# Optimization experiments

Measured on AMD Instinct MI355X. Metric: run time of the kernel, lower is better.

## Reference

```python
import jax, jax.numpy as jnp
import numpy as np

N_NODES = 100000
N_EDGES = 800000
IN_FEATS = 128
HIDDEN = 128
NUM_CLASSES = 10
NUM_GRAPHS = 128
BN_EPS = 1e-5


def setup_inputs() -> dict:
    key = jax.random.key(0)
    ks = jax.random.split(key, 16)
    s = 0.05  # weight init scale
    return {
        "x": jax.random.normal(ks[0], (N_NODES, IN_FEATS), dtype=jnp.float32),
        "edge_index": jax.random.randint(ks[1], (2, N_EDGES), 0, N_NODES, dtype=jnp.int64),
        "batch": jnp.sort(jax.random.randint(ks[2], (N_NODES,), 0, NUM_GRAPHS, dtype=jnp.int64)),
        # conv1 MLP: Linear(in,h) -> ReLU -> Linear(h,h)
        "W1a": jax.random.normal(ks[3], (IN_FEATS, HIDDEN), dtype=jnp.float32) * s,
        "b1a": jnp.zeros((HIDDEN,), dtype=jnp.float32),
        "W1b": jax.random.normal(ks[4], (HIDDEN, HIDDEN), dtype=jnp.float32) * s,
        "b1b": jnp.zeros((HIDDEN,), dtype=jnp.float32),
        "gamma1": jnp.ones((HIDDEN,), dtype=jnp.float32),
        "beta1": jnp.zeros((HIDDEN,), dtype=jnp.float32),
        # conv2 MLP
        "W2a": jax.random.normal(ks[5], (HIDDEN, HIDDEN), dtype=jnp.float32) * s,
        "b2a": jnp.zeros((HIDDEN,), dtype=jnp.float32),
        "W2b": jax.random.normal(ks[6], (HIDDEN, HIDDEN), dtype=jnp.float32) * s,
        "b2b": jnp.zeros((HIDDEN,), dtype=jnp.float32),
        "gamma2": jnp.ones((HIDDEN,), dtype=jnp.float32),
        "beta2": jnp.zeros((HIDDEN,), dtype=jnp.float32),
        # final classifier
        "Wlin": jax.random.normal(ks[7], (HIDDEN, NUM_CLASSES), dtype=jnp.float32) * s,
        "blin": jnp.zeros((NUM_CLASSES,), dtype=jnp.float32),
    }


def _gin_conv(x, edge_index, Wa, ba, Wb, bb, eps=0.0):
    # GINConv: MLP((1+eps)*x_i + sum_{j->i} x_j); scatter-add over edges
    src, dst = edge_index[0], edge_index[1]
    agg = jax.ops.segment_sum(x[src], dst, num_segments=N_NODES)
    h = (1.0 + eps) * x + agg
    h = jax.nn.relu(h @ Wa + ba) @ Wb + bb
    return h


def _batch_norm(x, gamma, beta):
    # training-mode BN over the node dim (biased variance, as in torch)
    mean = jnp.mean(x, axis=0)
    var = jnp.mean(jnp.square(x - mean), axis=0)
    return (x - mean) * jax.lax.rsqrt(var + BN_EPS) * gamma + beta


def reference(x, edge_index, batch, W1a, b1a, W1b, b1b, gamma1, beta1,
              W2a, b2a, W2b, b2b, gamma2, beta2, Wlin, blin):
    h = _gin_conv(x, edge_index, W1a, b1a, W1b, b1b)
    h = jax.nn.relu(_batch_norm(h, gamma1, beta1))
    # dropout: eval mode -> identity
    h = _gin_conv(h, edge_index, W2a, b2a, W2b, b2b)
    h = jax.nn.relu(_batch_norm(h, gamma2, beta2))
    # global mean pool per graph
    summed = jax.ops.segment_sum(h, batch, num_segments=NUM_GRAPHS)
    counts = jax.ops.segment_sum(jnp.ones((h.shape[0],), h.dtype), batch, num_segments=NUM_GRAPHS)
    pooled = summed / jnp.maximum(counts, 1.0)[:, None]  # [G, H]
    logits = pooled @ Wlin + blin
    return jax.nn.log_softmax(logits, axis=1)
```

## Files before the change

kernel.cpp:

```cpp
#include <hip/hip_runtime.h>

#define N_NODES 100000
#define N_EDGESC 800000
#define HID 128
#define NGRAPH 128
#define BN_EPS 1e-5f
#define NREP 32
#define PS 136
#define MLP_GRID 521

#define PBLK 256
#define PCHUNK 3125
#define NCOARSE 196
#define HISTN (NCOARSE * PBLK)
#define HSCAN_BLOCKS (HISTN / 1024)

typedef __bf16 bf16x8 __attribute__((ext_vector_type(8)));
typedef float f32x4 __attribute__((ext_vector_type(4)));

__device__ inline unsigned short f2bf(float f) {
    unsigned int u = __float_as_uint(f);
    unsigned int r = u + 0x7FFFu + ((u >> 16) & 1u);
    return (unsigned short)(r >> 16);
}
__device__ inline float b2f(unsigned short u) {
    return __uint_as_float(((unsigned int)u) << 16);
}


__global__ __launch_bounds__(256) void k_phist(const int* __restrict__ dst,
                                               int* __restrict__ hist)
{
    __shared__ int h[NCOARSE];
    if (threadIdx.x < NCOARSE) h[threadIdx.x] = 0;
    __syncthreads();
    int base = blockIdx.x * PCHUNK;
    for (int i = threadIdx.x; i < PCHUNK; i += 256)
        atomicAdd(&h[dst[base + i] >> 9], 1);
    __syncthreads();
    if (threadIdx.x < NCOARSE)
        hist[threadIdx.x * PBLK + blockIdx.x] = h[threadIdx.x];
}

__global__ __launch_bounds__(256) void k_scan_block(int* __restrict__ a,
    int* __restrict__ bsum, int n)
{
    __shared__ int ts[256];
    int base = blockIdx.x * 1024 + threadIdx.x * 4;
    int v[4], s = 0;
    #pragma unroll
    for (int i = 0; i < 4; ++i) {
        int idx = base + i;
        v[i] = (idx < n) ? a[idx] : 0;
        s += v[i];
    }
    ts[threadIdx.x] = s;
    __syncthreads();
    for (int d = 1; d < 256; d <<= 1) {
        int t = (threadIdx.x >= d) ? ts[threadIdx.x - d] : 0;
        __syncthreads();
        ts[threadIdx.x] += t;
        __syncthreads();
    }
    int run = ts[threadIdx.x] - s;
    #pragma unroll
    for (int i = 0; i < 4; ++i) {
        int idx = base + i;
        if (idx < n) a[idx] = run;
        run += v[i];
    }
    if (threadIdx.x == 255) bsum[blockIdx.x] = ts[255];
}

__global__ void k_scan_top(int* __restrict__ bsum, int nb)
{
    int run = 0;
    for (int i = 0; i < nb; ++i) { int t = bsum[i]; bsum[i] = run; run += t; }
}

__global__ __launch_bounds__(256) void k_scan_add(int* __restrict__ a,
    const int* __restrict__ bsum, int n)
{
    int i = blockIdx.x * 256 + threadIdx.x;
    if (i < n) a[i] += bsum[i >> 10];
}

__global__ __launch_bounds__(256) void k_pscatter(const int* __restrict__ src,
    const int* __restrict__ dst, const int* __restrict__ hist,
    unsigned int* __restrict__ pk1)
{
    __shared__ int cur[NCOARSE];
    if (threadIdx.x < NCOARSE)
        cur[threadIdx.x] = hist[threadIdx.x * PBLK + blockIdx.x];
    __syncthreads();
    int base = blockIdx.x * PCHUNK;
    for (int i = threadIdx.x; i < PCHUNK; i += 256) {
        int s = src[base + i], d = dst[base + i];
        int p = atomicAdd(&cur[d >> 9], 1);
        pk1[p] = ((unsigned int)s << 9) | (unsigned int)(d & 511);
    }
}

__global__ __launch_bounds__(256) void k_psort(const unsigned int* __restrict__ pk1,
    const int* __restrict__ hist, int* __restrict__ eidx, int* __restrict__ off)
{
    __shared__ int h[512], cur[512], ts[256];
    const int b = blockIdx.x;
    const int e0 = hist[b * PBLK];
    const int e1 = (b == NCOARSE - 1) ? N_EDGESC : hist[(b + 1) * PBLK];
    const int cnt = e1 - e0;
    h[threadIdx.x] = 0; h[threadIdx.x + 256] = 0;
    __syncthreads();
    for (int i = threadIdx.x; i < cnt; i += 256)
        atomicAdd(&h[pk1[e0 + i] & 511], 1);
    __syncthreads();
    int v0 = h[threadIdx.x * 2], v1 = h[threadIdx.x * 2 + 1];
    int s = v0 + v1;
    ts[threadIdx.x] = s;
    __syncthreads();
    for (int d = 1; d < 256; d <<= 1) {
        int t = (threadIdx.x >= d) ? ts[threadIdx.x - d] : 0;
        __syncthreads();
        ts[threadIdx.x] += t;
        __syncthreads();
    }
    int run = e0 + ts[threadIdx.x] - s;
    int n0 = b * 512 + threadIdx.x * 2;
    cur[threadIdx.x * 2]     = run;
    cur[threadIdx.x * 2 + 1] = run + v0;
    if (n0     <= N_NODES) off[n0]     = run;
    if (n0 + 1 <= N_NODES) off[n0 + 1] = run + v0;
    __syncthreads();
    for (int i = threadIdx.x; i < cnt; i += 256) {
        unsigned int u = pk1[e0 + i];
        int p = atomicAdd(&cur[u & 511], 1);
        eidx[p] = (int)(u >> 9);
    }
}

__global__ __launch_bounds__(256) void k_cvt(const float* __restrict__ X,
    unsigned short* __restrict__ Y, int n4)
{
    int i = blockIdx.x * 256 + threadIdx.x;
    if (i < n4) {
        float4 v = ((const float4*)X)[i];
        ((ushort4*)Y)[i] = make_ushort4(f2bf(v.x), f2bf(v.y), f2bf(v.z), f2bf(v.w));
    }
}

__global__ __launch_bounds__(256) void k_wcvt4(const float* __restrict__ Wa,
    const float* __restrict__ Wb, const float* __restrict__ Wc,
    const float* __restrict__ Wd, unsigned short* __restrict__ WT)
{
    int idx = blockIdx.x * 256 + threadIdx.x;
    int mat = idx >> 14, w = idx & 16383;
    int k = w >> 7, n = w & 127;
    const float* W = (mat == 0) ? Wa : (mat == 1) ? Wb : (mat == 2) ? Wc : Wd;
    WT[mat * 16384 + n * 128 + k] = f2bf(W[w]);
}

template<bool BN>
__device__ inline void acc_row(float* acc, uint4 v,
                               const float* sc, const float* sh)
{
    unsigned int u[4] = {v.x, v.y, v.z, v.w};
    #pragma unroll
    for (int j = 0; j < 4; ++j) {
        float lo = b2f((unsigned short)u[j]);
        float hi = b2f((unsigned short)(u[j] >> 16));
        if (BN) {
            lo = fmaxf(lo * sc[2*j]   + sh[2*j],   0.f);
            hi = fmaxf(hi * sc[2*j+1] + sh[2*j+1], 0.f);
        }
        acc[2*j]   += lo;
        acc[2*j+1] += hi;
    }
}

template<bool BN>
__global__ __launch_bounds__(256) void k_gather(
    const unsigned short* __restrict__ X, const float* __restrict__ SC,
    const int* __restrict__ off, const int* __restrict__ eidx,
    unsigned short* __restrict__ OUT, int M)
{
    int n = blockIdx.x * 16 + (threadIdx.x >> 4);
    if (n >= M) return;
    const int lane = threadIdx.x & 15;
    const size_t co = (size_t)lane * 8;

    float sc[8], sh[8];
    if (BN) {
        *(float4*)&sc[0] = ((const float4*)SC)[lane * 2];
        *(float4*)&sc[4] = ((const float4*)SC)[lane * 2 + 1];
        *(float4*)&sh[0] = ((const float4*)SC)[32 + lane * 2];
        *(float4*)&sh[4] = ((const float4*)SC)[32 + lane * 2 + 1];
    }

    float acc[8] = {0.f, 0.f, 0.f, 0.f, 0.f, 0.f, 0.f, 0.f};
    acc_row<BN>(acc, *(const uint4*)(X + (size_t)n * HID + co), sc, sh);

    int k = off[n], kend = off[n + 1];
    for (; k + 7 < kend; k += 8) {
        uint4 v0 = *(const uint4*)(X + (size_t)eidx[k]   * HID + co);
        uint4 v1 = *(const uint4*)(X + (size_t)eidx[k+1] * HID + co);
        uint4 v2 = *(const uint4*)(X + (size_t)eidx[k+2] * HID + co);
        uint4 v3 = *(const uint4*)(X + (size_t)eidx[k+3] * HID + co);
        uint4 v4 = *(const uint4*)(X + (size_t)eidx[k+4] * HID + co);
        uint4 v5 = *(const uint4*)(X + (size_t)eidx[k+5] * HID + co);
        uint4 v6 = *(const uint4*)(X + (size_t)eidx[k+6] * HID + co);
        uint4 v7 = *(const uint4*)(X + (size_t)eidx[k+7] * HID + co);
        acc_row<BN>(acc, v0, sc, sh); acc_row<BN>(acc, v1, sc, sh);
        acc_row<BN>(acc, v2, sc, sh); acc_row<BN>(acc, v3, sc, sh);
        acc_row<BN>(acc, v4, sc, sh); acc_row<BN>(acc, v5, sc, sh);
        acc_row<BN>(acc, v6, sc, sh); acc_row<BN>(acc, v7, sc, sh);
    }
    for (; k + 3 < kend; k += 4) {
        uint4 v0 = *(const uint4*)(X + (size_t)eidx[k]   * HID + co);
        uint4 v1 = *(const uint4*)(X + (size_t)eidx[k+1] * HID + co);
        uint4 v2 = *(const uint4*)(X + (size_t)eidx[k+2] * HID + co);
        uint4 v3 = *(const uint4*)(X + (size_t)eidx[k+3] * HID + co);
        acc_row<BN>(acc, v0, sc, sh); acc_row<BN>(acc, v1, sc, sh);
        acc_row<BN>(acc, v2, sc, sh); acc_row<BN>(acc, v3, sc, sh);
    }
    for (; k < kend; ++k) {
        uint4 v = *(const uint4*)(X + (size_t)eidx[k] * HID + co);
        acc_row<BN>(acc, v, sc, sh);
    }

    uint4 o;
    o.x = (unsigned int)f2bf(acc[0]) | ((unsigned int)f2bf(acc[1]) << 16);
    o.y = (unsigned int)f2bf(acc[2]) | ((unsigned int)f2bf(acc[3]) << 16);
    o.z = (unsigned int)f2bf(acc[4]) | ((unsigned int)f2bf(acc[5]) << 16);
    o.w = (unsigned int)f2bf(acc[6]) | ((unsigned int)f2bf(acc[7]) << 16);
    *(uint4*)(OUT + (size_t)n * HID + co) = o;
}

__global__ __launch_bounds__(256) void k_mlp(
    const unsigned short* __restrict__ A,
    const unsigned short* __restrict__ WTa, const float* __restrict__ ba,
    const unsigned short* __restrict__ WTb, const float* __restrict__ bb,
    unsigned short* __restrict__ Cb, float* __restrict__ Srep, int M)
{
    __shared__ unsigned short Hs[4][16 * PS];

    const int tid = threadIdx.x;
    const int wave = tid >> 6;
    const int lane = tid & 63;
    const int m = lane & 15;
    const int quad = lane >> 4;
    unsigned short* lds = Hs[wave];
    const int ntiles = (M + 63) / 64;

    float bav[8], bbv[8];
    #pragma unroll
    for (int n0 = 0; n0 < 8; ++n0) { bav[n0] = ba[n0*16+m]; bbv[n0] = bb[n0*16+m]; }

    float s[8] = {0,0,0,0,0,0,0,0}, s2[8] = {0,0,0,0,0,0,0,0};

    int t = blockIdx.x;
    bf16x8 aN[4];
    if (t < ntiles) {
        const unsigned short* arow = A + (size_t)(t*64 + wave*16 + m) * HID + quad*8;
        #pragma unroll
        for (int kk = 0; kk < 4; ++kk) aN[kk] = *(const bf16x8*)(arow + kk*32);
    }

    for (; t < ntiles; t += MLP_GRID) {
        bf16x8 a[4];
        #pragma unroll
        for (int kk = 0; kk < 4; ++kk) a[kk] = aN[kk];

        int tn = t + MLP_GRID;
        if (tn < ntiles) {
            const unsigned short* arow = A + (size_t)(tn*64 + wave*16 + m) * HID + quad*8;
            #pragma unroll
            for (int kk = 0; kk < 4; ++kk) aN[kk] = *(const bf16x8*)(arow + kk*32);
        }

        f32x4 acc[8];
        #pragma unroll
        for (int n0 = 0; n0 < 8; ++n0) acc[n0] = {0.f, 0.f, 0.f, 0.f};
        #pragma unroll
        for (int kk = 0; kk < 4; ++kk) {
            #pragma unroll
            for (int n0 = 0; n0 < 8; ++n0) {
                bf16x8 bv = *(const bf16x8*)(WTa + (size_t)(n0*16+m)*HID + quad*8 + kk*32);
                acc[n0] = __builtin_amdgcn_mfma_f32_16x16x32_bf16(a[kk], bv, acc[n0], 0, 0, 0);
            }
        }

        #pragma unroll
        for (int n0 = 0; n0 < 8; ++n0)
            #pragma unroll
            for (int r = 0; r < 4; ++r)
                lds[(quad*4+r)*PS + n0*16+m] = f2bf(fmaxf(acc[n0][r] + bav[n0], 0.f));
        __builtin_amdgcn_sched_barrier(0);

        bf16x8 hfr[4];
        #pragma unroll
        for (int kk = 0; kk < 4; ++kk)
            hfr[kk] = *(const bf16x8*)(lds + m*PS + quad*8 + kk*32);
        __builtin_amdgcn_sched_barrier(0);

        #pragma unroll
        for (int n0 = 0; n0 < 8; ++n0) acc[n0] = {0.f, 0.f, 0.f, 0.f};
        #pragma unroll
        for (int kk = 0; kk < 4; ++kk) {
            #pragma unroll
            for (int n0 = 0; n0 < 8; ++n0) {
                bf16x8 bv = *(const bf16x8*)(WTb + (size_t)(n0*16+m)*HID + quad*8 + kk*32);
                acc[n0] = __builtin_amdgcn_mfma_f32_16x16x32_bf16(hfr[kk], bv, acc[n0], 0, 0, 0);
            }
        }

        const int rowbase = t*64 + wave*16;
        bool full = (rowbase + 16 <= M);
        #pragma unroll
        for (int n0 = 0; n0 < 8; ++n0) {
            #pragma unroll
            for (int r = 0; r < 4; ++r) {
                float v = acc[n0][r] + bbv[n0];
                if (full || rowbase + quad*4 + r < M) { s[n0] += v; s2[n0] += v*v; }
                lds[(quad*4+r)*PS + n0*16+m] = f2bf(v);
            }
        }
        __builtin_amdgcn_sched_barrier(0);
        #pragma unroll
        for (int it = 0; it < 4; ++it) {
            int idx = it*64 + lane;
            int row = idx >> 4, chunk = idx & 15;
            uint4 v = *(const uint4*)(lds + row*PS + chunk*8);
            int g = rowbase + row;
            if (g < M) *(uint4*)(Cb + (size_t)g*HID + chunk*8) = v;
        }
        __builtin_amdgcn_sched_barrier(0);
    }

    #pragma unroll
    for (int n0 = 0; n0 < 8; ++n0) {
        s[n0]  += __shfl_xor(s[n0], 16, 64);
        s[n0]  += __shfl_xor(s[n0], 32, 64);
        s2[n0] += __shfl_xor(s2[n0], 16, 64);
        s2[n0] += __shfl_xor(s2[n0], 32, 64);
    }
    if (quad == 0) {
        float* R = Srep + (size_t)((blockIdx.x * 4 + wave) & (NREP - 1)) * 256;
        #pragma unroll
        for (int n0 = 0; n0 < 8; ++n0) {
            atomicAdd(&R[n0*16+m], s[n0]);
            atomicAdd(&R[128 + n0*16+m], s2[n0]);
        }
    }
}

__global__ void k_bnfinalize(const float* __restrict__ Srep,
    const float* __restrict__ gamma, const float* __restrict__ beta,
    float* __restrict__ SC, int M)
{
    int f = threadIdx.x;
    float s = 0.f, s2 = 0.f;
    for (int r = 0; r < NREP; ++r) {
        s += Srep[r * 256 + f];
        s2 += Srep[r * 256 + 128 + f];
    }
    float mean = s / (float)M;
    float var = s2 / (float)M - mean * mean;
    var = fmaxf(var, 0.f);
    float sc = gamma[f] * rsqrtf(var + BN_EPS);
    SC[f] = sc;
    SC[HID + f] = beta[f] - mean * sc;
}

__global__ void k_bounds(const int* __restrict__ batch, int* __restrict__ gstart)
{
    int g = threadIdx.x;
    int lo = 0, hi = N_NODES;
    while (lo < hi) {
        int mid = (lo + hi) >> 1;
        if (batch[mid] < g) lo = mid + 1; else hi = mid;
    }
    gstart[g] = lo;
    if (g == 0) gstart[NGRAPH] = N_NODES;
}

__global__ __launch_bounds__(256) void k_pool(const unsigned short* __restrict__ H,
    const float* __restrict__ SC, const int* __restrict__ gstart,
    float* __restrict__ P)
{
    int g = blockIdx.x >> 4, part = blockIdx.x & 15;
    int beg = gstart[g], end = gstart[g + 1];
    int f = threadIdx.x & 127, half = threadIdx.x >> 7;
    float sc = SC[f], sh = SC[HID + f];
    float s = 0.f;
    for (int r = beg + part * 2 + half; r < end; r += 32)
        s += fmaxf(b2f(H[(size_t)r * HID + f]) * sc + sh, 0.f);
    __shared__ float ls[256];
    ls[threadIdx.x] = s;
    __syncthreads();
    if (threadIdx.x < 128)
        atomicAdd(&P[g * HID + threadIdx.x], ls[threadIdx.x] + ls[threadIdx.x + 128]);
}

__global__ void k_head(const float* __restrict__ P, const int* __restrict__ gstart,
    const float* __restrict__ Wlin, const float* __restrict__ blin,
    float* __restrict__ out)
{
    int g = blockIdx.x;
    int l = threadIdx.x;
    float inv = 1.f / (float)max(gstart[g + 1] - gstart[g], 1);
    float p0 = P[(size_t)g * HID + l] * inv;
    float p1 = P[(size_t)g * HID + 64 + l] * inv;
    float lg[10];
    #pragma unroll
    for (int c = 0; c < 10; ++c) {
        float v = p0 * Wlin[l * 10 + c] + p1 * Wlin[(64 + l) * 10 + c];
        #pragma unroll
        for (int off = 32; off > 0; off >>= 1) v += __shfl_down(v, off);
        lg[c] = v;
    }
    if (l == 0) {
        float mx = -1e30f;
        #pragma unroll
        for (int c = 0; c < 10; ++c) { lg[c] += blin[c]; mx = fmaxf(mx, lg[c]); }
        float s = 0.f;
        #pragma unroll
        for (int c = 0; c < 10; ++c) s += expf(lg[c] - mx);
        float lse = mx + logf(s);
        #pragma unroll
        for (int c = 0; c < 10; ++c) out[g * 10 + c] = lg[c] - lse;
    }
}

extern "C" void kernel_launch(void* const* d_in, const int* in_sizes, int n_in,
                              void* d_out, int out_size, void* d_ws, size_t ws_size,
                              hipStream_t stream)
{
    const float* x    = (const float*)d_in[0];
    const int*   ei   = (const int*)d_in[1];
    const int*   batch= (const int*)d_in[2];
    const float* W1a  = (const float*)d_in[3];
    const float* b1a  = (const float*)d_in[4];
    const float* W1b  = (const float*)d_in[5];
    const float* b1b  = (const float*)d_in[6];
    const float* g1   = (const float*)d_in[7];
    const float* be1  = (const float*)d_in[8];
    const float* W2a  = (const float*)d_in[9];
    const float* b2a  = (const float*)d_in[10];
    const float* W2b  = (const float*)d_in[11];
    const float* b2b  = (const float*)d_in[12];
    const float* g2   = (const float*)d_in[13];
    const float* be2  = (const float*)d_in[14];
    const float* Wl   = (const float*)d_in[15];
    const float* bl   = (const float*)d_in[16];
    float* out = (float*)d_out;

    const int* src = ei;
    const int* dst = ei + N_EDGESC;

    const size_t NM = (size_t)N_NODES * HID;
    char* wsb = (char*)d_ws;
    unsigned short* Ab  = (unsigned short*)wsb;
    unsigned short* Yb  = Ab + NM;
    unsigned short* Xb  = Yb + NM;
    float* Srep1 = (float*)(Xb + NM);
    float* Srep2 = Srep1 + NREP * 256;
    float* SC1  = Srep2 + NREP * 256;
    float* SC2  = SC1 + 256;
    float* P    = SC2 + 256;
    unsigned short* WT = (unsigned short*)(P + (size_t)NGRAPH * HID);
    int* hist   = (int*)(WT + 4 * 16384);
    int* eidx   = hist + HISTN;
    int* off    = eidx + N_EDGESC;
    int* bsum   = off + N_NODES + 1;
    int* gstart = bsum + 64;
    unsigned int* pk1 = (unsigned int*)Xb;

    dim3 blk(256);
    const int cvtBlocks = (int)(NM / 4 + 255) / 256;
    const int gatBlocks = (N_NODES + 15) / 16;

    hipMemsetAsync(P, 0, (size_t)NGRAPH * HID * sizeof(float), stream);
    hipMemsetAsync(Srep1, 0, 2 * NREP * 256 * sizeof(float), stream);

    k_phist<<<PBLK, blk, 0, stream>>>(dst, hist);
    k_scan_block<<<HSCAN_BLOCKS, blk, 0, stream>>>(hist, bsum, HISTN);
    k_scan_top<<<1, 1, 0, stream>>>(bsum, HSCAN_BLOCKS);
    k_scan_add<<<(HISTN + 255) / 256, blk, 0, stream>>>(hist, bsum, HISTN);
    k_pscatter<<<PBLK, blk, 0, stream>>>(src, dst, hist, pk1);
    k_psort<<<NCOARSE, blk, 0, stream>>>(pk1, hist, eidx, off);
    k_bounds<<<1, 128, 0, stream>>>(batch, gstart);

    k_cvt<<<cvtBlocks, blk, 0, stream>>>(x, Xb, (int)(NM / 4));
    k_wcvt4<<<256, blk, 0, stream>>>(W1a, W1b, W2a, W2b, WT);

    k_gather<false><<<gatBlocks, blk, 0, stream>>>(Xb, nullptr, off, eidx, Ab, N_NODES);
    k_mlp<<<MLP_GRID, blk, 0, stream>>>(Ab, WT, b1a, WT + 16384, b1b, Yb, Srep1, N_NODES);
    k_bnfinalize<<<1, 128, 0, stream>>>(Srep1, g1, be1, SC1, N_NODES);

    k_gather<true><<<gatBlocks, blk, 0, stream>>>(Yb, SC1, off, eidx, Ab, N_NODES);
    k_mlp<<<MLP_GRID, blk, 0, stream>>>(Ab, WT + 2 * 16384, b2a, WT + 3 * 16384, b2b, Xb, Srep2, N_NODES);
    k_bnfinalize<<<1, 128, 0, stream>>>(Srep2, g2, be2, SC2, N_NODES);

    k_pool<<<NGRAPH * 16, blk, 0, stream>>>(Xb, SC2, gstart, P);
    k_head<<<NGRAPH, 64, 0, stream>>>(P, gstart, Wl, bl, out);
}
```

Before: 354.2 us.

## Keep MLP weight slices in registers and share row tiles through LDS

Rewrites the fused two-layer MLP kernel. The grid changes from a persistent 521-block loop to one 64-row tile per block. Each wave now keeps a 32-column slice of both weight matrices in registers, and the 64-row input tile and the hidden activations are shared through LDS with block barriers. The goal is to stop reloading the full weight matrices from global memory for every 16-row tile in every wave. In exchange it adds block-level syncs and doubles LDS use, and it drops the software prefetch of the next tile. The last partial tile loads A rows past M without a bounds check.

Result: faster. 309.5 us (-12.6%).

```diff
diff --git a/kernel.cpp b/kernel.cpp
--- a/kernel.cpp
+++ b/kernel.cpp
@@ -7,7 +7,7 @@
 #define BN_EPS 1e-5f
 #define NREP 32
 #define PS 136
-#define MLP_GRID 521
+#define MLP_BLOCKS ((N_NODES + 63) / 64)
 
 #define PBLK 256
 #define PCHUNK 3125
@@ -241,103 +241,109 @@
     const unsigned short* __restrict__ WTb, const float* __restrict__ bb,
     unsigned short* __restrict__ Cb, float* __restrict__ Srep, int M)
 {
-    __shared__ unsigned short Hs[4][16 * PS];
-
-    const int tid = threadIdx.x;
+    __shared__ unsigned short Abuf[64 * PS];
+    __shared__ unsigned short Hbuf[64 * PS];
+
+    const int tid  = threadIdx.x;
     const int wave = tid >> 6;
     const int lane = tid & 63;
-    const int m = lane & 15;
+    const int m    = lane & 15;
     const int quad = lane >> 4;
-    unsigned short* lds = Hs[wave];
-    const int ntiles = (M + 63) / 64;
-
-    float bav[8], bbv[8];
-    #pragma unroll
-    for (int n0 = 0; n0 < 8; ++n0) { bav[n0] = ba[n0*16+m]; bbv[n0] = bb[n0*16+m]; }
-
-    float s[8] = {0,0,0,0,0,0,0,0}, s2[8] = {0,0,0,0,0,0,0,0};
-
-    int t = blockIdx.x;
-    bf16x8 aN[4];
-    if (t < ntiles) {
-        const unsigned short* arow = A + (size_t)(t*64 + wave*16 + m) * HID + quad*8;
-        #pragma unroll
-        for (int kk = 0; kk < 4; ++kk) aN[kk] = *(const bf16x8*)(arow + kk*32);
-    }
-
-    for (; t < ntiles; t += MLP_GRID) {
-        bf16x8 a[4];
-        #pragma unroll
-        for (int kk = 0; kk < 4; ++kk) a[kk] = aN[kk];
-
-        int tn = t + MLP_GRID;
-        if (tn < ntiles) {
-            const unsigned short* arow = A + (size_t)(tn*64 + wave*16 + m) * HID + quad*8;
+    const int rowbase = blockIdx.x * 64;
+
+    bf16x8 WA[2][4], WB[2][4];
+    float bav[2], bbv[2];
+    #pragma unroll
+    for (int n0 = 0; n0 < 2; ++n0) {
+        const int col = (wave * 2 + n0) * 16 + m;
+        const size_t cb = (size_t)col * HID + quad * 8;
+        #pragma unroll
+        for (int kk = 0; kk < 4; ++kk) {
+            WA[n0][kk] = *(const bf16x8*)(WTa + cb + kk * 32);
+            WB[n0][kk] = *(const bf16x8*)(WTb + cb + kk * 32);
+        }
+        bav[n0] = ba[col];
+        bbv[n0] = bb[col];
+    }
+
+    {
+        const uint4* Ag = (const uint4*)(A + (size_t)rowbase * HID);
+        #pragma unroll
+        for (int i = 0; i < 4; ++i) {
+            int u = tid + i * 256;
+            uint4 v = Ag[u];
+            int r = u >> 4, c = u & 15;
+            *(uint4*)(Abuf + r * PS + c * 8) = v;
+        }
+    }
+    __syncthreads();
+
+    f32x4 acc[4][2];
+    #pragma unroll
+    for (int rg = 0; rg < 4; ++rg)
+        #pragma unroll
+        for (int n0 = 0; n0 < 2; ++n0) acc[rg][n0] = {0.f, 0.f, 0.f, 0.f};
+    #pragma unroll
+    for (int rg = 0; rg < 4; ++rg) {
+        #pragma unroll
+        for (int kk = 0; kk < 4; ++kk) {
+            bf16x8 af = *(const bf16x8*)(Abuf + (rg*16 + m) * PS + quad*8 + kk*32);
+            acc[rg][0] = __builtin_amdgcn_mfma_f32_16x16x32_bf16(af, WA[0][kk], acc[rg][0], 0, 0, 0);
+            acc[rg][1] = __builtin_amdgcn_mfma_f32_16x16x32_bf16(af, WA[1][kk], acc[rg][1], 0, 0, 0);
+        }
+    }
+
+    #pragma unroll
+    for (int rg = 0; rg < 4; ++rg)
+        #pragma unroll
+        for (int n0 = 0; n0 < 2; ++n0)
             #pragma unroll
-            for (int kk = 0; kk < 4; ++kk) aN[kk] = *(const bf16x8*)(arow + kk*32);
-        }
-
-        f32x4 acc[8];
-        #pragma unroll
-        for (int n0 = 0; n0 < 8; ++n0) acc[n0] = {0.f, 0.f, 0.f, 0.f};
+            for (int i = 0; i < 4; ++i)
+                Hbuf[(rg*16 + quad*4 + i) * PS + (wave*2 + n0)*16 + m] =
+                    f2bf(fmaxf(acc[rg][n0][i] + bav[n0], 0.f));
+    __syncthreads();
+
+    #pragma unroll
+    for (int rg = 0; rg < 4; ++rg)
+        #pragma unroll
+        for (int n0 = 0; n0 < 2; ++n0) acc[rg][n0] = {0.f, 0.f, 0.f, 0.f};
+    #pragma unroll
+    for (int rg = 0; rg < 4; ++rg) {
         #pragma unroll
         for (int kk = 0; kk < 4; ++kk) {
+            bf16x8 hf = *(const bf16x8*)(Hbuf + (rg*16 + m) * PS + quad*8 + kk*32);
+            acc[rg][0] = __builtin_amdgcn_mfma_f32_16x16x32_bf16(hf, WB[0][kk], acc[rg][0], 0, 0, 0);
+            acc[rg][1] = __builtin_amdgcn_mfma_f32_16x16x32_bf16(hf, WB[1][kk], acc[rg][1], 0, 0, 0);
+        }
+    }
+
+    const bool full = (rowbase + 64 <= M);
+    float s[2] = {0.f, 0.f}, s2[2] = {0.f, 0.f};
+    #pragma unroll
+    for (int rg = 0; rg < 4; ++rg) {
+        #pragma unroll
+        for (int n0 = 0; n0 < 2; ++n0) {
             #pragma unroll
-            for (int n0 = 0; n0 < 8; ++n0) {
-                bf16x8 bv = *(const bf16x8*)(WTa + (size_t)(n0*16+m)*HID + quad*8 + kk*32);
-                acc[n0] = __builtin_amdgcn_mfma_f32_16x16x32_bf16(a[kk], bv, acc[n0], 0, 0, 0);
+            for (int i = 0; i < 4; ++i) {
+                float v = acc[rg][n0][i] + bbv[n0];
+                if (full || rowbase + rg*16 + quad*4 + i < M) { s[n0] += v; s2[n0] += v*v; }
+                Abuf[(rg*16 + quad*4 + i) * PS + (wave*2 + n0)*16 + m] = f2bf(v);
             }
         }
-
-        #pragma unroll
-        for (int n0 = 0; n0 < 8; ++n0)
-            #pragma unroll
-            for (int r = 0; r < 4; ++r)
-                lds[(quad*4+r)*PS + n0*16+m] = f2bf(fmaxf(acc[n0][r] + bav[n0], 0.f));
-        __builtin_amdgcn_sched_barrier(0);
-
-        bf16x8 hfr[4];
-        #pragma unroll
-        for (int kk = 0; kk < 4; ++kk)
-            hfr[kk] = *(const bf16x8*)(lds + m*PS + quad*8 + kk*32);
-        __builtin_amdgcn_sched_barrier(0);
-
-        #pragma unroll
-        for (int n0 = 0; n0 < 8; ++n0) acc[n0] = {0.f, 0.f, 0.f, 0.f};
-        #pragma unroll
-        for (int kk = 0; kk < 4; ++kk) {
-            #pragma unroll
-            for (int n0 = 0; n0 < 8; ++n0) {
-                bf16x8 bv = *(const bf16x8*)(WTb + (size_t)(n0*16+m)*HID + quad*8 + kk*32);
-                acc[n0] = __builtin_amdgcn_mfma_f32_16x16x32_bf16(hfr[kk], bv, acc[n0], 0, 0, 0);
-            }
-        }
-
-        const int rowbase = t*64 + wave*16;
-        bool full = (rowbase + 16 <= M);
-        #pragma unroll
-        for (int n0 = 0; n0 < 8; ++n0) {
-            #pragma unroll
-            for (int r = 0; r < 4; ++r) {
-                float v = acc[n0][r] + bbv[n0];
-                if (full || rowbase + quad*4 + r < M) { s[n0] += v; s2[n0] += v*v; }
-                lds[(quad*4+r)*PS + n0*16+m] = f2bf(v);
-            }
-        }
-        __builtin_amdgcn_sched_barrier(0);
-        #pragma unroll
-        for (int it = 0; it < 4; ++it) {
-            int idx = it*64 + lane;
-            int row = idx >> 4, chunk = idx & 15;
-            uint4 v = *(const uint4*)(lds + row*PS + chunk*8);
-            int g = rowbase + row;
-            if (g < M) *(uint4*)(Cb + (size_t)g*HID + chunk*8) = v;
-        }
-        __builtin_amdgcn_sched_barrier(0);
-    }
-
-    #pragma unroll
-    for (int n0 = 0; n0 < 8; ++n0) {
+    }
+    __syncthreads();
+
+    #pragma unroll
+    for (int i = 0; i < 4; ++i) {
+        int u = tid + i * 256;
+        int r = u >> 4, c = u & 15;
+        uint4 v = *(const uint4*)(Abuf + r * PS + c * 8);
+        int g = rowbase + r;
+        if (g < M) *(uint4*)(Cb + (size_t)g * HID + c * 8) = v;
+    }
+
+    #pragma unroll
+    for (int n0 = 0; n0 < 2; ++n0) {
         s[n0]  += __shfl_xor(s[n0], 16, 64);
         s[n0]  += __shfl_xor(s[n0], 32, 64);
         s2[n0] += __shfl_xor(s2[n0], 16, 64);
@@ -346,9 +352,10 @@
     if (quad == 0) {
         float* R = Srep + (size_t)((blockIdx.x * 4 + wave) & (NREP - 1)) * 256;
         #pragma unroll
-        for (int n0 = 0; n0 < 8; ++n0) {
-            atomicAdd(&R[n0*16+m], s[n0]);
-            atomicAdd(&R[128 + n0*16+m], s2[n0]);
+        for (int n0 = 0; n0 < 2; ++n0) {
+            int col = (wave * 2 + n0) * 16 + m;
+            atomicAdd(&R[col], s[n0]);
+            atomicAdd(&R[128 + col], s2[n0]);
         }
     }
 }
@@ -494,11 +501,11 @@
     k_wcvt4<<<256, blk, 0, stream>>>(W1a, W1b, W2a, W2b, WT);
 
     k_gather<false><<<gatBlocks, blk, 0, stream>>>(Xb, nullptr, off, eidx, Ab, N_NODES);
-    k_mlp<<<MLP_GRID, blk, 0, stream>>>(Ab, WT, b1a, WT + 16384, b1b, Yb, Srep1, N_NODES);
+    k_mlp<<<MLP_BLOCKS, blk, 0, stream>>>(Ab, WT, b1a, WT + 16384, b1b, Yb, Srep1, N_NODES);
     k_bnfinalize<<<1, 128, 0, stream>>>(Srep1, g1, be1, SC1, N_NODES);
 
     k_gather<true><<<gatBlocks, blk, 0, stream>>>(Yb, SC1, off, eidx, Ab, N_NODES);
-    k_mlp<<<MLP_GRID, blk, 0, stream>>>(Ab, WT + 2 * 16384, b2a, WT + 3 * 16384, b2b, Xb, Srep2, N_NODES);
+    k_mlp<<<MLP_BLOCKS, blk, 0, stream>>>(Ab, WT + 2 * 16384, b2a, WT + 3 * 16384, b2b, Xb, Srep2, N_NODES);
     k_bnfinalize<<<1, 128, 0, stream>>>(Srep2, g2, be2, SC2, N_NODES);
 
     k_pool<<<NGRAPH * 16, blk, 0, stream>>>(Xb, SC2, gstart, P);
```
